# Optimization experiments

Measured on AMD Instinct MI355X. Metric: run time of the kernel, lower is better.

The kernel has to match this reference:

```python
import jax, jax.numpy as jnp
import numpy as np

N = 1024
OBS_RADIUS = 0.5


def setup_inputs() -> dict:
    key = jax.random.key(0)
    ks = jax.random.split(key, 16)
    def w(k, shape, fan_in):
        return jax.random.normal(k, shape, dtype=jnp.float32) / np.sqrt(fan_in).astype(np.float32)
    return {
        "s": jax.random.normal(ks[0], (N, 4), dtype=jnp.float32),
        "g": jax.random.normal(ks[1], (N, 2), dtype=jnp.float32),
        "conv1_w": w(ks[2], (64, 5), 5),   "conv1_b": jnp.zeros((64,), jnp.float32),
        "conv2_w": w(ks[3], (128, 64), 64), "conv2_b": jnp.zeros((128,), jnp.float32),
        "fc1_w": w(ks[4], (64, 132), 132), "fc1_b": jnp.zeros((64,), jnp.float32),
        "fc2_w": w(ks[5], (128, 64), 64),  "fc2_b": jnp.zeros((128,), jnp.float32),
        "fc3_w": w(ks[6], (64, 128), 128), "fc3_b": jnp.zeros((64,), jnp.float32),
        "fc4_w": w(ks[7], (4, 64), 64),    "fc4_b": jnp.zeros((4,), jnp.float32),
    }


def reference(s, g, conv1_w, conv1_b, conv2_w, conv2_b,
              fc1_w, fc1_b, fc2_w, fc2_b, fc3_w, fc3_b, fc4_w, fc4_b):
    n = s.shape[0]
    # pairwise agent diff + identity channel: [n, n, 5]
    pd = s[:, None, :] - s[None, :, :]
    x = jnp.concatenate([pd, jnp.eye(n, dtype=s.dtype)[:, :, None]], axis=2)
    # neighbor mask from positional distance: [n, n, 1]
    dist = jnp.linalg.norm(x[:, :, :2], axis=2, keepdims=True)
    mask = (dist < OBS_RADIUS).astype(s.dtype)
    # 1x1-conv edge MLPs (pointwise over the j dim): [n, n, 64] -> [n, n, 128]
    h = jax.nn.relu(jnp.einsum('ijc,oc->ijo', x, conv1_w) + conv1_b)
    h = jax.nn.relu(jnp.einsum('ijc,oc->ijo', h, conv2_w) + conv2_b)
    # masked max-pool over neighbors j: [n, 128]
    pooled = jnp.max(h * mask, axis=1)
    sg = s[:, :2] - g
    feat = jnp.concatenate([pooled, sg, s[:, 2:]], axis=1)  # [n, 132]
    z = jax.nn.relu(feat @ fc1_w.T + fc1_b)
    z = jax.nn.relu(z @ fc2_w.T + fc2_b)
    z = jax.nn.relu(z @ fc3_w.T + fc3_b)
    k = 2.0 * jax.nn.sigmoid(z @ fc4_w.T + fc4_b) - 1.0  # [n, 4]
    k1, k2, k3, k4 = k[:, 0:1], k[:, 1:2], k[:, 2:3], k[:, 3:4]
    zr = jnp.zeros_like(k1)
    gain_x = -jnp.concatenate([k1, zr, k2, zr], axis=1)
    gain_y = -jnp.concatenate([zr, k3, zr, k4], axis=1)
    state = jnp.concatenate([sg, s[:, 2:]], axis=1)  # [n, 4]
    a_x = jnp.sum(state * gain_x, axis=1, keepdims=True)
    a_y = jnp.sum(state * gain_y, axis=1, keepdims=True)
    return jnp.concatenate([a_x, a_y], axis=1)  # [n, 2]
```

## Files before the change

### kernel.cpp

```cpp
#include <hip/hip_runtime.h>

typedef unsigned int u32;
typedef unsigned short u16;
typedef _Float16 f16;
typedef f16 f16x8 __attribute__((ext_vector_type(8)));
typedef float f32x4 __attribute__((ext_vector_type(4)));

#define NTH 256
#define SH1 72

__global__ __launch_bounds__(NTH) void NetworkAction_86131274154571_kernel(
    const float* __restrict__ s,    const float* __restrict__ g,
    const float* __restrict__ w1g,  const float* __restrict__ b1g,
    const float* __restrict__ w2g,  const float* __restrict__ b2g,
    const float* __restrict__ fc1w, const float* __restrict__ fc1b,
    const float* __restrict__ fc2w, const float* __restrict__ fc2b,
    const float* __restrict__ fc3w, const float* __restrict__ fc3b,
    const float* __restrict__ fc4w, const float* __restrict__ fc4b,
    float2* __restrict__ out)
{
    __shared__ float4 acts[1024];
    __shared__ int    actj[1024];
    __shared__ f16    h1buf[16][SH1];
    __shared__ float  w1s[320];
    __shared__ float  b1s[64];
    __shared__ float  feat[132];
    __shared__ float  z1[64];
    __shared__ float  z2[128];
    __shared__ float  z3[64];
    __shared__ float  kk[4];
    __shared__ int    cnt;

    const int tid  = threadIdx.x;
    const int lane = tid & 63;
    const int wave = tid >> 6;
    const int i    = blockIdx.x;

    if (tid == 0) cnt = 0;
    for (int q = tid; q < 320; q += NTH) w1s[q] = w1g[q];
    if (tid < 64) b1s[tid] = b1g[tid];
    __syncthreads();

    const float4 si = ((const float4*)s)[i];

    #pragma unroll
    for (int p = 0; p < 4; ++p) {
        const int j = p * NTH + tid;
        float4 sj = ((const float4*)s)[j];
        float dx = si.x - sj.x, dy = si.y - sj.y;
        if (dx * dx + dy * dy < 0.25f) {
            int slot = atomicAdd(&cnt, 1);
            acts[slot] = sj;
            actj[slot] = j;
        }
    }
    __syncthreads();
    const int n_act = cnt;

    const int n_base = wave * 32;
    const int ncol   = lane & 15;
    const int kq     = lane >> 4;
    f16x8 bfrag[2][2];
    float b2r[2];
    #pragma unroll
    for (int tile = 0; tile < 2; ++tile) {
        const int n = n_base + tile * 16 + ncol;
        b2r[tile] = b2g[n];
        #pragma unroll
        for (int t = 0; t < 2; ++t) {
            const float* wp = w2g + n * 64 + t * 32 + kq * 8;
            float4 lo = ((const float4*)wp)[0];
            float4 hi = ((const float4*)wp)[1];
            f16x8 b;
            b[0] = (f16)lo.x; b[1] = (f16)lo.y; b[2] = (f16)lo.z; b[3] = (f16)lo.w;
            b[4] = (f16)hi.x; b[5] = (f16)hi.y; b[6] = (f16)hi.z; b[7] = (f16)hi.w;
            bfrag[tile][t] = b;
        }
    }

    float mtile[2] = {0.0f, 0.0f};

    for (int gbase = 0; gbase < n_act; gbase += 16) {
        #pragma unroll
        for (int it = 0; it < 2; ++it) {
            const int idx = it * NTH + tid;
            const int p = idx >> 5, c2 = idx & 31;
            if (gbase + p < n_act) {
                const float4 sj = acts[gbase + p];
                const float x0 = si.x - sj.x, x1 = si.y - sj.y;
                const float x2 = si.z - sj.z, x3 = si.w - sj.w;
                const float x4 = (actj[gbase + p] == i) ? 1.0f : 0.0f;
                const int c = c2 * 2;
                const float* wa = &w1s[c * 5];
                float ha = b1s[c];
                ha = fmaf(wa[0], x0, ha); ha = fmaf(wa[1], x1, ha);
                ha = fmaf(wa[2], x2, ha); ha = fmaf(wa[3], x3, ha);
                ha = fmaf(wa[4], x4, ha);
                const float* wb = &w1s[c * 5 + 5];
                float hb = b1s[c + 1];
                hb = fmaf(wb[0], x0, hb); hb = fmaf(wb[1], x1, hb);
                hb = fmaf(wb[2], x2, hb); hb = fmaf(wb[3], x3, hb);
                hb = fmaf(wb[4], x4, hb);
                f16 fa = (f16)fmaxf(ha, 0.0f);
                f16 fb = (f16)fmaxf(hb, 0.0f);
                u32 pk = (u32)__builtin_bit_cast(u16, fa) |
                         ((u32)__builtin_bit_cast(u16, fb) << 16);
                *(u32*)&h1buf[p][c2 * 2] = pk;
            }
        }
        __syncthreads();

        f16x8 afr[2];
        #pragma unroll
        for (int t = 0; t < 2; ++t)
            afr[t] = *(const f16x8*)&h1buf[ncol][t * 32 + kq * 8];

        #pragma unroll
        for (int tile = 0; tile < 2; ++tile) {
            f32x4 acc = {0.0f, 0.0f, 0.0f, 0.0f};
            acc = __builtin_amdgcn_mfma_f32_16x16x32_f16(afr[0], bfrag[tile][0], acc, 0, 0, 0);
            acc = __builtin_amdgcn_mfma_f32_16x16x32_f16(afr[1], bfrag[tile][1], acc, 0, 0, 0);
            #pragma unroll
            for (int r = 0; r < 4; ++r) {
                const bool valid = (gbase + kq * 4 + r) < n_act;
                const float v = acc[r] + b2r[tile];
                mtile[tile] = valid ? fmaxf(mtile[tile], v) : mtile[tile];
            }
        }
        __syncthreads();
    }

    #pragma unroll
    for (int tile = 0; tile < 2; ++tile) {
        float m = mtile[tile];
        m = fmaxf(m, __shfl_xor(m, 16));
        m = fmaxf(m, __shfl_xor(m, 32));
        if (lane < 16) feat[n_base + tile * 16 + lane] = m;
    }
    if (tid == 0) {
        float2 gi = ((const float2*)g)[i];
        feat[128] = si.x - gi.x;
        feat[129] = si.y - gi.y;
        feat[130] = si.z;
        feat[131] = si.w;
    }
    __syncthreads();

    if (tid < 64) {
        float acc = fc1b[tid];
        const float4* wv = (const float4*)(fc1w + tid * 132);
        #pragma unroll
        for (int q = 0; q < 33; ++q) {
            float4 u = wv[q];
            int k = q * 4;
            acc = fmaf(u.x, feat[k+0], acc);
            acc = fmaf(u.y, feat[k+1], acc);
            acc = fmaf(u.z, feat[k+2], acc);
            acc = fmaf(u.w, feat[k+3], acc);
        }
        z1[tid] = fmaxf(acc, 0.0f);
    }
    __syncthreads();

    if (tid < 128) {
        float acc = fc2b[tid];
        const float4* wv = (const float4*)(fc2w + tid * 64);
        #pragma unroll
        for (int q = 0; q < 16; ++q) {
            float4 u = wv[q];
            int k = q * 4;
            acc = fmaf(u.x, z1[k+0], acc);
            acc = fmaf(u.y, z1[k+1], acc);
            acc = fmaf(u.z, z1[k+2], acc);
            acc = fmaf(u.w, z1[k+3], acc);
        }
        z2[tid] = fmaxf(acc, 0.0f);
    }
    __syncthreads();

    if (tid < 64) {
        float acc = fc3b[tid];
        const float4* wv = (const float4*)(fc3w + tid * 128);
        #pragma unroll
        for (int q = 0; q < 32; ++q) {
            float4 u = wv[q];
            int k = q * 4;
            acc = fmaf(u.x, z2[k+0], acc);
            acc = fmaf(u.y, z2[k+1], acc);
            acc = fmaf(u.z, z2[k+2], acc);
            acc = fmaf(u.w, z2[k+3], acc);
        }
        z3[tid] = fmaxf(acc, 0.0f);
    }
    __syncthreads();

    if (tid < 4) {
        float acc = fc4b[tid];
        const float4* wv = (const float4*)(fc4w + tid * 64);
        #pragma unroll
        for (int q = 0; q < 16; ++q) {
            float4 u = wv[q];
            int k = q * 4;
            acc = fmaf(u.x, z3[k+0], acc);
            acc = fmaf(u.y, z3[k+1], acc);
            acc = fmaf(u.z, z3[k+2], acc);
            acc = fmaf(u.w, z3[k+3], acc);
        }
        kk[tid] = 2.0f / (1.0f + expf(-acc)) - 1.0f;
    }
    __syncthreads();

    if (tid == 0) {
        float ax = -(kk[0] * feat[128] + kk[1] * feat[130]);
        float ay = -(kk[2] * feat[129] + kk[3] * feat[131]);
        out[i] = make_float2(ax, ay);
    }
}

extern "C" void kernel_launch(void* const* d_in, const int* in_sizes, int n_in,
                              void* d_out, int out_size, void* d_ws, size_t ws_size,
                              hipStream_t stream) {
    const float* s    = (const float*)d_in[0];
    const float* g    = (const float*)d_in[1];
    const float* c1w  = (const float*)d_in[2];
    const float* c1b  = (const float*)d_in[3];
    const float* c2w  = (const float*)d_in[4];
    const float* c2b  = (const float*)d_in[5];
    const float* fc1w = (const float*)d_in[6];
    const float* fc1b = (const float*)d_in[7];
    const float* fc2w = (const float*)d_in[8];
    const float* fc2b = (const float*)d_in[9];
    const float* fc3w = (const float*)d_in[10];
    const float* fc3b = (const float*)d_in[11];
    const float* fc4w = (const float*)d_in[12];
    const float* fc4b = (const float*)d_in[13];

    float2* out = (float2*)d_out;

    NetworkAction_86131274154571_kernel<<<1024, NTH, 0, stream>>>(
        s, g, c1w, c1b, c2w, c2b, fc1w, fc1b, fc2w, fc2b,
        fc3w, fc3b, fc4w, fc4b, out);
}
```

Measured before the change: 95.78 us.

## Split pooling and MLP head into two kernels; batch head via MFMA

The per-row MLP head moves out of the pooling kernel into a second kernel. That kernel handles 32 rows per block and runs the four FC layers as f16 MFMA matmuls with weights staged in shared memory. Pooled features pass between the kernels through workspace memory as f16. The aim is to stop running serial scalar GEMVs with long weight reloads in every one of the 1024 blocks. The cost is an extra launch, a workspace round trip, and lower precision in the head.

```diff
diff --git a/kernel.cpp b/kernel.cpp
--- a/kernel.cpp
+++ b/kernel.cpp
@@ -9,26 +9,22 @@
 #define NTH 256
 #define SH1 72
 
-__global__ __launch_bounds__(NTH) void NetworkAction_86131274154571_kernel(
-    const float* __restrict__ s,    const float* __restrict__ g,
-    const float* __restrict__ w1g,  const float* __restrict__ b1g,
-    const float* __restrict__ w2g,  const float* __restrict__ b2g,
-    const float* __restrict__ fc1w, const float* __restrict__ fc1b,
-    const float* __restrict__ fc2w, const float* __restrict__ fc2b,
-    const float* __restrict__ fc3w, const float* __restrict__ fc3b,
-    const float* __restrict__ fc4w, const float* __restrict__ fc4b,
-    float2* __restrict__ out)
+__device__ __forceinline__ u32 pack2(float a, float b) {
+    f16 fa = (f16)a, fb = (f16)b;
+    return (u32)__builtin_bit_cast(u16, fa) | ((u32)__builtin_bit_cast(u16, fb) << 16);
+}
+
+__global__ __launch_bounds__(NTH) void pool_kernel(
+    const float* __restrict__ s,
+    const float* __restrict__ w1g, const float* __restrict__ b1g,
+    const float* __restrict__ w2g, const float* __restrict__ b2g,
+    u16* __restrict__ pooled)
 {
     __shared__ float4 acts[1024];
     __shared__ int    actj[1024];
     __shared__ f16    h1buf[16][SH1];
     __shared__ float  w1s[320];
     __shared__ float  b1s[64];
-    __shared__ float  feat[132];
-    __shared__ float  z1[64];
-    __shared__ float  z2[128];
-    __shared__ float  z3[64];
-    __shared__ float  kk[4];
     __shared__ int    cnt;
 
     const int tid  = threadIdx.x;
@@ -101,11 +97,7 @@
                 hb = fmaf(wb[0], x0, hb); hb = fmaf(wb[1], x1, hb);
                 hb = fmaf(wb[2], x2, hb); hb = fmaf(wb[3], x3, hb);
                 hb = fmaf(wb[4], x4, hb);
-                f16 fa = (f16)fmaxf(ha, 0.0f);
-                f16 fb = (f16)fmaxf(hb, 0.0f);
-                u32 pk = (u32)__builtin_bit_cast(u16, fa) |
-                         ((u32)__builtin_bit_cast(u16, fb) << 16);
-                *(u32*)&h1buf[p][c2 * 2] = pk;
+                *(u32*)&h1buf[p][c2 * 2] = pack2(fmaxf(ha, 0.0f), fmaxf(hb, 0.0f));
             }
         }
         __syncthreads();
@@ -135,85 +127,186 @@
         float m = mtile[tile];
         m = fmaxf(m, __shfl_xor(m, 16));
         m = fmaxf(m, __shfl_xor(m, 32));
-        if (lane < 16) feat[n_base + tile * 16 + lane] = m;
-    }
-    if (tid == 0) {
-        float2 gi = ((const float2*)g)[i];
-        feat[128] = si.x - gi.x;
-        feat[129] = si.y - gi.y;
-        feat[130] = si.z;
-        feat[131] = si.w;
-    }
-    __syncthreads();
-
-    if (tid < 64) {
-        float acc = fc1b[tid];
-        const float4* wv = (const float4*)(fc1w + tid * 132);
-        #pragma unroll
-        for (int q = 0; q < 33; ++q) {
-            float4 u = wv[q];
-            int k = q * 4;
-            acc = fmaf(u.x, feat[k+0], acc);
-            acc = fmaf(u.y, feat[k+1], acc);
-            acc = fmaf(u.z, feat[k+2], acc);
-            acc = fmaf(u.w, feat[k+3], acc);
-        }
-        z1[tid] = fmaxf(acc, 0.0f);
-    }
-    __syncthreads();
-
-    if (tid < 128) {
-        float acc = fc2b[tid];
-        const float4* wv = (const float4*)(fc2w + tid * 64);
-        #pragma unroll
-        for (int q = 0; q < 16; ++q) {
-            float4 u = wv[q];
-            int k = q * 4;
-            acc = fmaf(u.x, z1[k+0], acc);
-            acc = fmaf(u.y, z1[k+1], acc);
-            acc = fmaf(u.z, z1[k+2], acc);
-            acc = fmaf(u.w, z1[k+3], acc);
-        }
-        z2[tid] = fmaxf(acc, 0.0f);
-    }
-    __syncthreads();
-
-    if (tid < 64) {
-        float acc = fc3b[tid];
-        const float4* wv = (const float4*)(fc3w + tid * 128);
-        #pragma unroll
-        for (int q = 0; q < 32; ++q) {
-            float4 u = wv[q];
-            int k = q * 4;
-            acc = fmaf(u.x, z2[k+0], acc);
-            acc = fmaf(u.y, z2[k+1], acc);
-            acc = fmaf(u.z, z2[k+2], acc);
-            acc = fmaf(u.w, z2[k+3], acc);
-        }
-        z3[tid] = fmaxf(acc, 0.0f);
-    }
-    __syncthreads();
-
-    if (tid < 4) {
-        float acc = fc4b[tid];
-        const float4* wv = (const float4*)(fc4w + tid * 64);
-        #pragma unroll
-        for (int q = 0; q < 16; ++q) {
-            float4 u = wv[q];
-            int k = q * 4;
-            acc = fmaf(u.x, z3[k+0], acc);
-            acc = fmaf(u.y, z3[k+1], acc);
-            acc = fmaf(u.z, z3[k+2], acc);
-            acc = fmaf(u.w, z3[k+3], acc);
-        }
-        kk[tid] = 2.0f / (1.0f + expf(-acc)) - 1.0f;
-    }
-    __syncthreads();
-
-    if (tid == 0) {
-        float ax = -(kk[0] * feat[128] + kk[1] * feat[130]);
-        float ay = -(kk[2] * feat[129] + kk[3] * feat[131]);
-        out[i] = make_float2(ax, ay);
+        if (lane < 16) {
+            f16 h = (f16)m;
+            pooled[i * 128 + n_base + tile * 16 + lane] = __builtin_bit_cast(u16, h);
+        }
+    }
+}
+
+__global__ __launch_bounds__(NTH) void head_kernel(
+    const float* __restrict__ s,    const float* __restrict__ g,
+    const float* __restrict__ fc1w, const float* __restrict__ fc1b,
+    const float* __restrict__ fc2w, const float* __restrict__ fc2b,
+    const float* __restrict__ fc3w, const float* __restrict__ fc3b,
+    const float* __restrict__ fc4w, const float* __restrict__ fc4b,
+    const u16* __restrict__ pooled,
+    float2* __restrict__ out)
+{
+    __shared__ f16 feat[32][168];
+    __shared__ f16 w1s[64][168];
+    __shared__ f16 z1s[32][72];
+    __shared__ f16 w2s[128][72];
+    __shared__ f16 z2s[32][136];
+    __shared__ f16 w3s[64][136];
+    __shared__ f16 z3s[32][72];
+    __shared__ f16 w4s[16][72];
+    __shared__ float b1h[64], b2h[128], b3h[64], b4h[4];
+    __shared__ float kbuf[32][4];
+
+    const int tid  = threadIdx.x;
+    const int lane = tid & 63;
+    const int wave = tid >> 6;
+    const int r0   = blockIdx.x * 32;
+
+    for (int slot = tid; slot < 64 * 66; slot += NTH) {
+        int n = slot / 66, kp = slot % 66;
+        float2 v = *(const float2*)(fc1w + n * 132 + kp * 2);
+        *(u32*)&w1s[n][kp * 2] = pack2(v.x, v.y);
+    }
+    for (int slot = tid; slot < 128 * 32; slot += NTH) {
+        int n = slot / 32, kp = slot % 32;
+        float2 v = *(const float2*)(fc2w + n * 64 + kp * 2);
+        *(u32*)&w2s[n][kp * 2] = pack2(v.x, v.y);
+    }
+    for (int slot = tid; slot < 64 * 64; slot += NTH) {
+        int n = slot / 64, kp = slot % 64;
+        float2 v = *(const float2*)(fc3w + n * 128 + kp * 2);
+        *(u32*)&w3s[n][kp * 2] = pack2(v.x, v.y);
+    }
+    for (int slot = tid; slot < 4 * 32; slot += NTH) {
+        int n = slot / 32, kp = slot % 32;
+        float2 v = *(const float2*)(fc4w + n * 64 + kp * 2);
+        *(u32*)&w4s[n][kp * 2] = pack2(v.x, v.y);
+    }
+    for (int slot = tid; slot < 12 * 32; slot += NTH) {
+        int n = 4 + slot / 32, kp = slot % 32;
+        *(u32*)&w4s[n][kp * 2] = 0;
+    }
+    for (int slot = tid; slot < 32 * 64; slot += NTH) {
+        int r = slot / 64, kp = slot % 64;
+        *(u32*)&feat[r][kp * 2] = ((const u32*)(pooled + (r0 + r) * 128))[kp];
+    }
+    if (tid < 32) {
+        int r = r0 + tid;
+        float4 sv = ((const float4*)s)[r];
+        float2 gv = ((const float2*)g)[r];
+        *(u32*)&feat[tid][128] = pack2(sv.x - gv.x, sv.y - gv.y);
+        *(u32*)&feat[tid][130] = pack2(sv.z, sv.w);
+    }
+    for (int slot = tid; slot < 32 * 14; slot += NTH) {
+        int r = slot / 14, kp = slot % 14;
+        *(u32*)&feat[r][132 + kp * 2] = 0;
+    }
+    for (int slot = tid; slot < 64 * 14; slot += NTH) {
+        int n = slot / 14, kp = slot % 14;
+        *(u32*)&w1s[n][132 + kp * 2] = 0;
+    }
+    if (tid < 64)  b1h[tid] = fc1b[tid];
+    if (tid < 128) b2h[tid] = fc2b[tid];
+    if (tid < 64)  b3h[tid] = fc3b[tid];
+    if (tid < 4)   b4h[tid] = fc4b[tid];
+    __syncthreads();
+
+    const int mt = wave >> 1, nh = wave & 1;
+    const int m0 = mt * 16;
+    const int lr = lane & 15, kq = lane >> 4;
+
+    {
+        f16x8 a[5];
+        #pragma unroll
+        for (int ks = 0; ks < 5; ++ks)
+            a[ks] = *(const f16x8*)&feat[m0 + lr][ks * 32 + kq * 8];
+        #pragma unroll
+        for (int nt = 0; nt < 2; ++nt) {
+            const int ntile = nh * 2 + nt;
+            f32x4 acc = {0.0f, 0.0f, 0.0f, 0.0f};
+            #pragma unroll
+            for (int ks = 0; ks < 5; ++ks) {
+                f16x8 b = *(const f16x8*)&w1s[ntile * 16 + lr][ks * 32 + kq * 8];
+                acc = __builtin_amdgcn_mfma_f32_16x16x32_f16(a[ks], b, acc, 0, 0, 0);
+            }
+            const int n = ntile * 16 + lr;
+            const float bn = b1h[n];
+            #pragma unroll
+            for (int r = 0; r < 4; ++r)
+                z1s[m0 + kq * 4 + r][n] = (f16)fmaxf(acc[r] + bn, 0.0f);
+        }
+    }
+    __syncthreads();
+
+    {
+        f16x8 a[2];
+        #pragma unroll
+        for (int ks = 0; ks < 2; ++ks)
+            a[ks] = *(const f16x8*)&z1s[m0 + lr][ks * 32 + kq * 8];
+        #pragma unroll
+        for (int nt = 0; nt < 4; ++nt) {
+            const int ntile = nh * 4 + nt;
+            f32x4 acc = {0.0f, 0.0f, 0.0f, 0.0f};
+            #pragma unroll
+            for (int ks = 0; ks < 2; ++ks) {
+                f16x8 b = *(const f16x8*)&w2s[ntile * 16 + lr][ks * 32 + kq * 8];
+                acc = __builtin_amdgcn_mfma_f32_16x16x32_f16(a[ks], b, acc, 0, 0, 0);
+            }
+            const int n = ntile * 16 + lr;
+            const float bn = b2h[n];
+            #pragma unroll
+            for (int r = 0; r < 4; ++r)
+                z2s[m0 + kq * 4 + r][n] = (f16)fmaxf(acc[r] + bn, 0.0f);
+        }
+    }
+    __syncthreads();
+
+    {
+        f16x8 a[4];
+        #pragma unroll
+        for (int ks = 0; ks < 4; ++ks)
+            a[ks] = *(const f16x8*)&z2s[m0 + lr][ks * 32 + kq * 8];
+        #pragma unroll
+        for (int nt = 0; nt < 2; ++nt) {
+            const int ntile = nh * 2 + nt;
+            f32x4 acc = {0.0f, 0.0f, 0.0f, 0.0f};
+            #pragma unroll
+            for (int ks = 0; ks < 4; ++ks) {
+                f16x8 b = *(const f16x8*)&w3s[ntile * 16 + lr][ks * 32 + kq * 8];
+                acc = __builtin_amdgcn_mfma_f32_16x16x32_f16(a[ks], b, acc, 0, 0, 0);
+            }
+            const int n = ntile * 16 + lr;
+            const float bn = b3h[n];
+            #pragma unroll
+            for (int r = 0; r < 4; ++r)
+                z3s[m0 + kq * 4 + r][n] = (f16)fmaxf(acc[r] + bn, 0.0f);
+        }
+    }
+    __syncthreads();
+
+    {
+        f16x8 a0 = *(const f16x8*)&z3s[m0 + lr][kq * 8];
+        f16x8 a1 = *(const f16x8*)&z3s[m0 + lr][32 + kq * 8];
+        f16x8 b0 = *(const f16x8*)&w4s[lr][kq * 8];
+        f16x8 b1 = *(const f16x8*)&w4s[lr][32 + kq * 8];
+        f32x4 acc = {0.0f, 0.0f, 0.0f, 0.0f};
+        acc = __builtin_amdgcn_mfma_f32_16x16x32_f16(a0, b0, acc, 0, 0, 0);
+        acc = __builtin_amdgcn_mfma_f32_16x16x32_f16(a1, b1, acc, 0, 0, 0);
+        if (nh == 0 && lr < 4) {
+            const float bn = b4h[lr];
+            #pragma unroll
+            for (int r = 0; r < 4; ++r)
+                kbuf[m0 + kq * 4 + r][lr] =
+                    2.0f / (1.0f + expf(-(acc[r] + bn))) - 1.0f;
+        }
+    }
+    __syncthreads();
+
+    if (tid < 32) {
+        int r = r0 + tid;
+        float4 sv = ((const float4*)s)[r];
+        float2 gv = ((const float2*)g)[r];
+        float sgx = sv.x - gv.x, sgy = sv.y - gv.y;
+        float ax = -(kbuf[tid][0] * sgx + kbuf[tid][1] * sv.z);
+        float ay = -(kbuf[tid][2] * sgy + kbuf[tid][3] * sv.w);
+        out[r] = make_float2(ax, ay);
     }
 }
 
@@ -235,9 +328,10 @@
     const float* fc4w = (const float*)d_in[12];
     const float* fc4b = (const float*)d_in[13];
 
+    u16* pooled = (u16*)d_ws;
     float2* out = (float2*)d_out;
 
-    NetworkAction_86131274154571_kernel<<<1024, NTH, 0, stream>>>(
-        s, g, c1w, c1b, c2w, c2b, fc1w, fc1b, fc2w, fc2b,
-        fc3w, fc3b, fc4w, fc4b, out);
+    pool_kernel<<<1024, NTH, 0, stream>>>(s, c1w, c1b, c2w, c2b, pooled);
+    head_kernel<<<32, NTH, 0, stream>>>(s, g, fc1w, fc1b, fc2w, fc2b,
+                                        fc3w, fc3b, fc4w, fc4b, pooled, out);
 }
```

After: 102.5 us. +7.0%, slower.

## Process two agents per block with 512 threads and double-buffered edge tiles

Applied to the files above, without the earlier changes.

Each block now handles two agents i with 512 threads, so 8 waves each own one 16-column MFMA tile. Neighbor filtering for both agents happens in a single pass over s, which is staged once in LDS and indexed by compact u16 lists. The h1 staging buffer is double-buffered, which removes one barrier per 16-neighbor group. The launch is halved to 512 blocks. Because the two agents' neighbor loops run sequentially, per-block latency grows, and only 512 blocks may underfill the GPU.

```diff
diff --git a/kernel.cpp b/kernel.cpp
--- a/kernel.cpp
+++ b/kernel.cpp
@@ -6,8 +6,13 @@
 typedef f16 f16x8 __attribute__((ext_vector_type(8)));
 typedef float f32x4 __attribute__((ext_vector_type(4)));
 
-#define NTH 256
+#define NTH 512
 #define SH1 72
+
+__device__ __forceinline__ u32 pack2(float a, float b) {
+    f16 fa = (f16)a, fb = (f16)b;
+    return (u32)__builtin_bit_cast(u16, fa) | ((u32)__builtin_bit_cast(u16, fb) << 16);
+}
 
 __global__ __launch_bounds__(NTH) void NetworkAction_86131274154571_kernel(
     const float* __restrict__ s,    const float* __restrict__ g,
@@ -19,53 +24,49 @@
     const float* __restrict__ fc4w, const float* __restrict__ fc4b,
     float2* __restrict__ out)
 {
-    __shared__ float4 acts[1024];
-    __shared__ int    actj[1024];
-    __shared__ f16    h1buf[16][SH1];
+    __shared__ float4 slds[1024];
+    __shared__ u16    idx[2][1024];
+    __shared__ int    cnt[2];
+    __shared__ f16    h1buf[2][16][SH1];
     __shared__ float  w1s[320];
     __shared__ float  b1s[64];
-    __shared__ float  feat[132];
-    __shared__ float  z1[64];
-    __shared__ float  z2[128];
-    __shared__ float  z3[64];
-    __shared__ float  kk[4];
-    __shared__ int    cnt;
+    __shared__ float  feat[2][132];
+    __shared__ float  z1[2][64];
+    __shared__ float  z2[2][128];
+    __shared__ float  z3[2][64];
+    __shared__ float  kk[2][4];
 
     const int tid  = threadIdx.x;
     const int lane = tid & 63;
     const int wave = tid >> 6;
-    const int i    = blockIdx.x;
-
-    if (tid == 0) cnt = 0;
-    for (int q = tid; q < 320; q += NTH) w1s[q] = w1g[q];
-    if (tid < 64) b1s[tid] = b1g[tid];
-    __syncthreads();
-
-    const float4 si = ((const float4*)s)[i];
+    const int i0   = blockIdx.x * 2;
+
+    if (tid < 2) cnt[tid] = 0;
+    if (tid < 320) w1s[tid] = w1g[tid];
+    else if (tid >= 448) b1s[tid - 448] = b1g[tid - 448];
+
+    const float4 si0 = ((const float4*)s)[i0];
+    const float4 si1 = ((const float4*)s)[i0 + 1];
+    __syncthreads();
 
     #pragma unroll
-    for (int p = 0; p < 4; ++p) {
+    for (int p = 0; p < 2; ++p) {
         const int j = p * NTH + tid;
         float4 sj = ((const float4*)s)[j];
-        float dx = si.x - sj.x, dy = si.y - sj.y;
-        if (dx * dx + dy * dy < 0.25f) {
-            int slot = atomicAdd(&cnt, 1);
-            acts[slot] = sj;
-            actj[slot] = j;
-        }
-    }
-    __syncthreads();
-    const int n_act = cnt;
-
-    const int n_base = wave * 32;
-    const int ncol   = lane & 15;
-    const int kq     = lane >> 4;
-    f16x8 bfrag[2][2];
-    float b2r[2];
-    #pragma unroll
-    for (int tile = 0; tile < 2; ++tile) {
-        const int n = n_base + tile * 16 + ncol;
-        b2r[tile] = b2g[n];
+        slds[j] = sj;
+        float dx0 = si0.x - sj.x, dy0 = si0.y - sj.y;
+        if (dx0 * dx0 + dy0 * dy0 < 0.25f)
+            idx[0][atomicAdd(&cnt[0], 1)] = (u16)j;
+        float dx1 = si1.x - sj.x, dy1 = si1.y - sj.y;
+        if (dx1 * dx1 + dy1 * dy1 < 0.25f)
+            idx[1][atomicAdd(&cnt[1], 1)] = (u16)j;
+    }
+
+    const int lr = lane & 15;
+    const int kq = lane >> 4;
+    const int n  = wave * 16 + lr;
+    f16x8 bfrag[2];
+    {
         #pragma unroll
         for (int t = 0; t < 2; ++t) {
             const float* wp = w2g + n * 64 + t * 32 + kq * 8;
@@ -74,22 +75,27 @@
             f16x8 b;
             b[0] = (f16)lo.x; b[1] = (f16)lo.y; b[2] = (f16)lo.z; b[3] = (f16)lo.w;
             b[4] = (f16)hi.x; b[5] = (f16)hi.y; b[6] = (f16)hi.z; b[7] = (f16)hi.w;
-            bfrag[tile][t] = b;
-        }
-    }
-
-    float mtile[2] = {0.0f, 0.0f};
-
-    for (int gbase = 0; gbase < n_act; gbase += 16) {
-        #pragma unroll
-        for (int it = 0; it < 2; ++it) {
-            const int idx = it * NTH + tid;
-            const int p = idx >> 5, c2 = idx & 31;
-            if (gbase + p < n_act) {
-                const float4 sj = acts[gbase + p];
+            bfrag[t] = b;
+        }
+    }
+    const float b2r = b2g[n];
+    __syncthreads();
+
+    int buf = 0;
+    for (int r = 0; r < 2; ++r) {
+        const int i_r = i0 + r;
+        const float4 si = (r == 0) ? si0 : si1;
+        const int nact = cnt[r];
+        float m = 0.0f;
+
+        for (int gb = 0; gb < nact; gb += 16) {
+            const int p = tid >> 5, c2 = tid & 31;
+            if (gb + p < nact) {
+                const int j = idx[r][gb + p];
+                const float4 sj = slds[j];
                 const float x0 = si.x - sj.x, x1 = si.y - sj.y;
                 const float x2 = si.z - sj.z, x3 = si.w - sj.w;
-                const float x4 = (actj[gbase + p] == i) ? 1.0f : 0.0f;
+                const float x4 = (j == i_r) ? 1.0f : 0.0f;
                 const int c = c2 * 2;
                 const float* wa = &w1s[c * 5];
                 float ha = b1s[c];
@@ -101,119 +107,112 @@
                 hb = fmaf(wb[0], x0, hb); hb = fmaf(wb[1], x1, hb);
                 hb = fmaf(wb[2], x2, hb); hb = fmaf(wb[3], x3, hb);
                 hb = fmaf(wb[4], x4, hb);
-                f16 fa = (f16)fmaxf(ha, 0.0f);
-                f16 fb = (f16)fmaxf(hb, 0.0f);
-                u32 pk = (u32)__builtin_bit_cast(u16, fa) |
-                         ((u32)__builtin_bit_cast(u16, fb) << 16);
-                *(u32*)&h1buf[p][c2 * 2] = pk;
+                *(u32*)&h1buf[buf][p][c2 * 2] = pack2(fmaxf(ha, 0.0f), fmaxf(hb, 0.0f));
             }
-        }
-        __syncthreads();
-
-        f16x8 afr[2];
-        #pragma unroll
-        for (int t = 0; t < 2; ++t)
-            afr[t] = *(const f16x8*)&h1buf[ncol][t * 32 + kq * 8];
-
-        #pragma unroll
-        for (int tile = 0; tile < 2; ++tile) {
+            __syncthreads();
+
+            f16x8 a0 = *(const f16x8*)&h1buf[buf][lr][kq * 8];
+            f16x8 a1 = *(const f16x8*)&h1buf[buf][lr][32 + kq * 8];
             f32x4 acc = {0.0f, 0.0f, 0.0f, 0.0f};
-            acc = __builtin_amdgcn_mfma_f32_16x16x32_f16(afr[0], bfrag[tile][0], acc, 0, 0, 0);
-            acc = __builtin_amdgcn_mfma_f32_16x16x32_f16(afr[1], bfrag[tile][1], acc, 0, 0, 0);
+            acc = __builtin_amdgcn_mfma_f32_16x16x32_f16(a0, bfrag[0], acc, 0, 0, 0);
+            acc = __builtin_amdgcn_mfma_f32_16x16x32_f16(a1, bfrag[1], acc, 0, 0, 0);
             #pragma unroll
-            for (int r = 0; r < 4; ++r) {
-                const bool valid = (gbase + kq * 4 + r) < n_act;
-                const float v = acc[r] + b2r[tile];
-                mtile[tile] = valid ? fmaxf(mtile[tile], v) : mtile[tile];
+            for (int rs = 0; rs < 4; ++rs) {
+                const bool valid = (gb + kq * 4 + rs) < nact;
+                const float v = acc[rs] + b2r;
+                m = valid ? fmaxf(m, v) : m;
             }
-        }
-        __syncthreads();
-    }
-
-    #pragma unroll
-    for (int tile = 0; tile < 2; ++tile) {
-        float m = mtile[tile];
+            buf ^= 1;
+        }
+
         m = fmaxf(m, __shfl_xor(m, 16));
         m = fmaxf(m, __shfl_xor(m, 32));
-        if (lane < 16) feat[n_base + tile * 16 + lane] = m;
-    }
-    if (tid == 0) {
-        float2 gi = ((const float2*)g)[i];
-        feat[128] = si.x - gi.x;
-        feat[129] = si.y - gi.y;
-        feat[130] = si.z;
-        feat[131] = si.w;
-    }
-    __syncthreads();
-
-    if (tid < 64) {
-        float acc = fc1b[tid];
-        const float4* wv = (const float4*)(fc1w + tid * 132);
+        if (lane < 16) feat[r][n] = m;
+    }
+
+    if (tid < 2) {
+        const int i_r = i0 + tid;
+        const float4 sv = (tid == 0) ? si0 : si1;
+        float2 gv = ((const float2*)g)[i_r];
+        feat[tid][128] = sv.x - gv.x;
+        feat[tid][129] = sv.y - gv.y;
+        feat[tid][130] = sv.z;
+        feat[tid][131] = sv.w;
+    }
+    __syncthreads();
+
+    if (tid < 128) {
+        const int row = tid >> 6, c = tid & 63;
+        float acc = fc1b[c];
+        const float4* wv = (const float4*)(fc1w + c * 132);
         #pragma unroll
         for (int q = 0; q < 33; ++q) {
             float4 u = wv[q];
             int k = q * 4;
-            acc = fmaf(u.x, feat[k+0], acc);
-            acc = fmaf(u.y, feat[k+1], acc);
-            acc = fmaf(u.z, feat[k+2], acc);
-            acc = fmaf(u.w, feat[k+3], acc);
-        }
-        z1[tid] = fmaxf(acc, 0.0f);
+            acc = fmaf(u.x, feat[row][k+0], acc);
+            acc = fmaf(u.y, feat[row][k+1], acc);
+            acc = fmaf(u.z, feat[row][k+2], acc);
+            acc = fmaf(u.w, feat[row][k+3], acc);
+        }
+        z1[row][c] = fmaxf(acc, 0.0f);
+    }
+    __syncthreads();
+
+    if (tid < 256) {
+        const int row = tid >> 7, c = tid & 127;
+        float acc = fc2b[c];
+        const float4* wv = (const float4*)(fc2w + c * 64);
+        #pragma unroll
+        for (int q = 0; q < 16; ++q) {
+            float4 u = wv[q];
+            int k = q * 4;
+            acc = fmaf(u.x, z1[row][k+0], acc);
+            acc = fmaf(u.y, z1[row][k+1], acc);
+            acc = fmaf(u.z, z1[row][k+2], acc);
+            acc = fmaf(u.w, z1[row][k+3], acc);
+        }
+        z2[row][c] = fmaxf(acc, 0.0f);
     }
     __syncthreads();
 
     if (tid < 128) {
-        float acc = fc2b[tid];
-        const float4* wv = (const float4*)(fc2w + tid * 64);
+        const int row = tid >> 6, c = tid & 63;
+        float acc = fc3b[c];
+        const float4* wv = (const float4*)(fc3w + c * 128);
+        #pragma unroll
+        for (int q = 0; q < 32; ++q) {
+            float4 u = wv[q];
+            int k = q * 4;
+            acc = fmaf(u.x, z2[row][k+0], acc);
+            acc = fmaf(u.y, z2[row][k+1], acc);
+            acc = fmaf(u.z, z2[row][k+2], acc);
+            acc = fmaf(u.w, z2[row][k+3], acc);
+        }
+        z3[row][c] = fmaxf(acc, 0.0f);
+    }
+    __syncthreads();
+
+    if (tid < 8) {
+        const int row = tid >> 2, mi = tid & 3;
+        float acc = fc4b[mi];
+        const float4* wv = (const float4*)(fc4w + mi * 64);
         #pragma unroll
         for (int q = 0; q < 16; ++q) {
             float4 u = wv[q];
             int k = q * 4;
-            acc = fmaf(u.x, z1[k+0], acc);
-            acc = fmaf(u.y, z1[k+1], acc);
-            acc = fmaf(u.z, z1[k+2], acc);
-            acc = fmaf(u.w, z1[k+3], acc);
-        }
-        z2[tid] = fmaxf(acc, 0.0f);
-    }
-    __syncthreads();
-
-    if (tid < 64) {
-        float acc = fc3b[tid];
-        const float4* wv = (const float4*)(fc3w + tid * 128);
-        #pragma unroll
-        for (int q = 0; q < 32; ++q) {
-            float4 u = wv[q];
-            int k = q * 4;
-            acc = fmaf(u.x, z2[k+0], acc);
-            acc = fmaf(u.y, z2[k+1], acc);
-            acc = fmaf(u.z, z2[k+2], acc);
-            acc = fmaf(u.w, z2[k+3], acc);
-        }
-        z3[tid] = fmaxf(acc, 0.0f);
-    }
-    __syncthreads();
-
-    if (tid < 4) {
-        float acc = fc4b[tid];
-        const float4* wv = (const float4*)(fc4w + tid * 64);
-        #pragma unroll
-        for (int q = 0; q < 16; ++q) {
-            float4 u = wv[q];
-            int k = q * 4;
-            acc = fmaf(u.x, z3[k+0], acc);
-            acc = fmaf(u.y, z3[k+1], acc);
-            acc = fmaf(u.z, z3[k+2], acc);
-            acc = fmaf(u.w, z3[k+3], acc);
-        }
-        kk[tid] = 2.0f / (1.0f + expf(-acc)) - 1.0f;
-    }
-    __syncthreads();
-
-    if (tid == 0) {
-        float ax = -(kk[0] * feat[128] + kk[1] * feat[130]);
-        float ay = -(kk[2] * feat[129] + kk[3] * feat[131]);
-        out[i] = make_float2(ax, ay);
+            acc = fmaf(u.x, z3[row][k+0], acc);
+            acc = fmaf(u.y, z3[row][k+1], acc);
+            acc = fmaf(u.z, z3[row][k+2], acc);
+            acc = fmaf(u.w, z3[row][k+3], acc);
+        }
+        kk[row][mi] = 2.0f / (1.0f + expf(-acc)) - 1.0f;
+    }
+    __syncthreads();
+
+    if (tid < 2) {
+        float ax = -(kk[tid][0] * feat[tid][128] + kk[tid][1] * feat[tid][130]);
+        float ay = -(kk[tid][2] * feat[tid][129] + kk[tid][3] * feat[tid][131]);
+        out[i0 + tid] = make_float2(ax, ay);
     }
 }
 
@@ -237,7 +236,7 @@
 
     float2* out = (float2*)d_out;
 
-    NetworkAction_86131274154571_kernel<<<1024, NTH, 0, stream>>>(
+    NetworkAction_86131274154571_kernel<<<512, NTH, 0, stream>>>(
         s, g, c1w, c1b, c2w, c2b, fc1w, fc1b, fc2w, fc2b,
         fc3w, fc3b, fc4w, fc4b, out);
 }
```

Result: slower. 98.36 us (+2.7%).

## Double-buffer edge features, process 32 neighbors per step, store neighbor indices only

Applied to the files above, without the earlier changes.

The neighbor compaction now stores only 16-bit indices in shared memory and re-reads s from global/L2 for each neighbor, which shrinks LDS use and should raise occupancy. Each loop step now processes 32 neighbors with a double-buffered h1 tile, so one barrier per step replaces two. The w2 fragment load is moved ahead of the compaction so its latency overlaps it. In exchange, each neighbor's s row is fetched once per channel-pair thread, and small neighbor counts waste more padded work in a 32-row step.

```diff
diff --git a/kernel.cpp b/kernel.cpp
--- a/kernel.cpp
+++ b/kernel.cpp
@@ -8,6 +8,11 @@
 
 #define NTH 256
 #define SH1 72
+
+__device__ __forceinline__ u32 pack2(float a, float b) {
+    f16 fa = (f16)a, fb = (f16)b;
+    return (u32)__builtin_bit_cast(u16, fa) | ((u32)__builtin_bit_cast(u16, fb) << 16);
+}
 
 __global__ __launch_bounds__(NTH) void NetworkAction_86131274154571_kernel(
     const float* __restrict__ s,    const float* __restrict__ g,
@@ -19,17 +24,16 @@
     const float* __restrict__ fc4w, const float* __restrict__ fc4b,
     float2* __restrict__ out)
 {
-    __shared__ float4 acts[1024];
-    __shared__ int    actj[1024];
-    __shared__ f16    h1buf[16][SH1];
-    __shared__ float  w1s[320];
-    __shared__ float  b1s[64];
-    __shared__ float  feat[132];
-    __shared__ float  z1[64];
-    __shared__ float  z2[128];
-    __shared__ float  z3[64];
-    __shared__ float  kk[4];
-    __shared__ int    cnt;
+    __shared__ u16   idx[1024];
+    __shared__ f16   h1buf[2][32][SH1];
+    __shared__ float w1s[320];
+    __shared__ float b1s[64];
+    __shared__ int   cnt;
+    __shared__ float feat[132];
+    __shared__ float z1[64];
+    __shared__ float z2[128];
+    __shared__ float z3[64];
+    __shared__ float kk[4];
 
     const int tid  = threadIdx.x;
     const int lane = tid & 63;
@@ -39,23 +43,8 @@
     if (tid == 0) cnt = 0;
     for (int q = tid; q < 320; q += NTH) w1s[q] = w1g[q];
     if (tid < 64) b1s[tid] = b1g[tid];
-    __syncthreads();
 
     const float4 si = ((const float4*)s)[i];
-
-    #pragma unroll
-    for (int p = 0; p < 4; ++p) {
-        const int j = p * NTH + tid;
-        float4 sj = ((const float4*)s)[j];
-        float dx = si.x - sj.x, dy = si.y - sj.y;
-        if (dx * dx + dy * dy < 0.25f) {
-            int slot = atomicAdd(&cnt, 1);
-            acts[slot] = sj;
-            actj[slot] = j;
-        }
-    }
-    __syncthreads();
-    const int n_act = cnt;
 
     const int n_base = wave * 32;
     const int ncol   = lane & 15;
@@ -77,57 +66,67 @@
             bfrag[tile][t] = b;
         }
     }
+    __syncthreads();
+
+    #pragma unroll
+    for (int p = 0; p < 4; ++p) {
+        const int j = p * NTH + tid;
+        float4 sj = ((const float4*)s)[j];
+        float dx = si.x - sj.x, dy = si.y - sj.y;
+        if (dx * dx + dy * dy < 0.25f)
+            idx[atomicAdd(&cnt, 1)] = (u16)j;
+    }
+    __syncthreads();
+    const int nact = cnt;
 
     float mtile[2] = {0.0f, 0.0f};
 
-    for (int gbase = 0; gbase < n_act; gbase += 16) {
-        #pragma unroll
-        for (int it = 0; it < 2; ++it) {
-            const int idx = it * NTH + tid;
-            const int p = idx >> 5, c2 = idx & 31;
-            if (gbase + p < n_act) {
-                const float4 sj = acts[gbase + p];
+    int buf = 0;
+    for (int gb = 0; gb < nact; gb += 32) {
+        #pragma unroll
+        for (int it = 0; it < 4; ++it) {
+            const int item = it * NTH + tid;
+            const int p = item >> 5, c2 = item & 31;
+            if (gb + p < nact) {
+                const int j = idx[gb + p];
+                const float4 sj = ((const float4*)s)[j];
                 const float x0 = si.x - sj.x, x1 = si.y - sj.y;
                 const float x2 = si.z - sj.z, x3 = si.w - sj.w;
-                const float x4 = (actj[gbase + p] == i) ? 1.0f : 0.0f;
+                const float x4 = (j == i) ? 1.0f : 0.0f;
                 const int c = c2 * 2;
                 const float* wa = &w1s[c * 5];
                 float ha = b1s[c];
                 ha = fmaf(wa[0], x0, ha); ha = fmaf(wa[1], x1, ha);
                 ha = fmaf(wa[2], x2, ha); ha = fmaf(wa[3], x3, ha);
                 ha = fmaf(wa[4], x4, ha);
-                const float* wb = &w1s[c * 5 + 5];
+                const float* wb = wa + 5;
                 float hb = b1s[c + 1];
                 hb = fmaf(wb[0], x0, hb); hb = fmaf(wb[1], x1, hb);
                 hb = fmaf(wb[2], x2, hb); hb = fmaf(wb[3], x3, hb);
                 hb = fmaf(wb[4], x4, hb);
-                f16 fa = (f16)fmaxf(ha, 0.0f);
-                f16 fb = (f16)fmaxf(hb, 0.0f);
-                u32 pk = (u32)__builtin_bit_cast(u16, fa) |
-                         ((u32)__builtin_bit_cast(u16, fb) << 16);
-                *(u32*)&h1buf[p][c2 * 2] = pk;
+                *(u32*)&h1buf[buf][p][c2 * 2] = pack2(fmaxf(ha, 0.0f), fmaxf(hb, 0.0f));
             }
         }
         __syncthreads();
 
-        f16x8 afr[2];
-        #pragma unroll
-        for (int t = 0; t < 2; ++t)
-            afr[t] = *(const f16x8*)&h1buf[ncol][t * 32 + kq * 8];
-
-        #pragma unroll
-        for (int tile = 0; tile < 2; ++tile) {
-            f32x4 acc = {0.0f, 0.0f, 0.0f, 0.0f};
-            acc = __builtin_amdgcn_mfma_f32_16x16x32_f16(afr[0], bfrag[tile][0], acc, 0, 0, 0);
-            acc = __builtin_amdgcn_mfma_f32_16x16x32_f16(afr[1], bfrag[tile][1], acc, 0, 0, 0);
+        #pragma unroll
+        for (int ph = 0; ph < 2; ++ph) {
+            f16x8 a0 = *(const f16x8*)&h1buf[buf][ph * 16 + ncol][kq * 8];
+            f16x8 a1 = *(const f16x8*)&h1buf[buf][ph * 16 + ncol][32 + kq * 8];
             #pragma unroll
-            for (int r = 0; r < 4; ++r) {
-                const bool valid = (gbase + kq * 4 + r) < n_act;
-                const float v = acc[r] + b2r[tile];
-                mtile[tile] = valid ? fmaxf(mtile[tile], v) : mtile[tile];
+            for (int tile = 0; tile < 2; ++tile) {
+                f32x4 acc = {0.0f, 0.0f, 0.0f, 0.0f};
+                acc = __builtin_amdgcn_mfma_f32_16x16x32_f16(a0, bfrag[tile][0], acc, 0, 0, 0);
+                acc = __builtin_amdgcn_mfma_f32_16x16x32_f16(a1, bfrag[tile][1], acc, 0, 0, 0);
+                #pragma unroll
+                for (int r = 0; r < 4; ++r) {
+                    const bool valid = (gb + ph * 16 + kq * 4 + r) < nact;
+                    const float v = acc[r] + b2r[tile];
+                    mtile[tile] = valid ? fmaxf(mtile[tile], v) : mtile[tile];
+                }
             }
         }
-        __syncthreads();
+        buf ^= 1;
     }
 
     #pragma unroll
@@ -138,9 +137,9 @@
         if (lane < 16) feat[n_base + tile * 16 + lane] = m;
     }
     if (tid == 0) {
-        float2 gi = ((const float2*)g)[i];
-        feat[128] = si.x - gi.x;
-        feat[129] = si.y - gi.y;
+        float2 gv = ((const float2*)g)[i];
+        feat[128] = si.x - gv.x;
+        feat[129] = si.y - gv.y;
         feat[130] = si.z;
         feat[131] = si.w;
     }
```

Measured after the change: 100.6 us. 5.0% more time.
